# Kernel optimization log

Hardware: AMD Instinct MI355X
Metric: run time of the kernel (lower is better)

The kernel has to match this reference:

```python
import jax, jax.numpy as jnp
import numpy as np

D = 1024
D_H = 64

def setup_inputs() -> dict:
    key = jax.random.key(0)
    kx, kq, kk, kv = jax.random.split(key, 4)
    B, T = 4, 4096
    x = jax.random.normal(kx, (B, T, D), dtype=jnp.float32)
    # nn.Linear(d, d_H, bias=False) weights, stored as [d, d_H] (already transposed)
    s = 1.0 / np.sqrt(D)
    Wq = jax.random.uniform(kq, (D, D_H), dtype=jnp.float32, minval=-s, maxval=s)
    Wk = jax.random.uniform(kk, (D, D_H), dtype=jnp.float32, minval=-s, maxval=s)
    Wv = jax.random.uniform(kv, (D, D_H), dtype=jnp.float32, minval=-s, maxval=s)
    return {"x": x, "Wq": Wq, "Wk": Wk, "Wv": Wv}

def reference(x, Wq, Wk, Wv):
    B, T, d = x.shape
    Q = jnp.einsum('btd,dh->bth', x, Wq)
    K = jnp.einsum('btd,dh->bth', x, Wk)
    V = jnp.einsum('btd,dh->bth', x, Wv)
    # NOTE: original scales by self.d ** -0.5 (model dim), not d_H
    scores = jnp.einsum('bqh,bkh->bqk', Q, K) * (d ** -0.5)
    causal = jnp.tril(jnp.ones((T, T), dtype=bool))  # [T, T]
    scores = jnp.where(causal, scores, -jnp.inf)
    attn = jax.nn.softmax(scores, axis=-1)
    return jnp.einsum('bqk,bkh->bqh', attn, V)
```

## Files before the change

kernel.cpp:

```cpp
#include <hip/hip_runtime.h>
#include <hip/hip_bf16.h>

#define D_MODEL 1024
#define D_HEAD  64
#define T_SEQ   4096
#define NB      4
#define NROWS   (NB * T_SEQ)
#define SPLIT   8

typedef float f32x4 __attribute__((ext_vector_type(4)));
typedef __bf16 bf16x8 __attribute__((ext_vector_type(8)));
typedef unsigned short u16;

__device__ inline unsigned pk_bf16(float a, float b) {
    unsigned ua = __builtin_bit_cast(unsigned, a);
    unsigned ub = __builtin_bit_cast(unsigned, b);
    ua = (ua + 0x7FFFu + ((ua >> 16) & 1u)) >> 16;
    ub = (ub + 0x7FFFu + ((ub >> 16) & 1u)) >> 16;
    return ua | (ub << 16);
}
__device__ inline u16 bf16r(float a) {
    unsigned ua = __builtin_bit_cast(unsigned, a);
    return (u16)((ua + 0x7FFFu + ((ua >> 16) & 1u)) >> 16);
}

__global__ __launch_bounds__(256) void packw_kernel(
    const float* __restrict__ Wq, const float* __restrict__ Wk,
    const float* __restrict__ Wv, unsigned* __restrict__ Wpk)
{
    const int id = blockIdx.x * 256 + threadIdx.x;
    const int kb = id / 192;
    const int n  = id - kb * 192;
    const int sel = n >> 6, col = n & 63;
    const float* W = sel == 0 ? Wq : (sel == 1 ? Wk : Wv);
    float f[8];
#pragma unroll
    for (int j = 0; j < 8; ++j) f[j] = W[(kb * 8 + j) * 64 + col];
    uint4 o;
    o.x = pk_bf16(f[0], f[1]); o.y = pk_bf16(f[2], f[3]);
    o.z = pk_bf16(f[4], f[5]); o.w = pk_bf16(f[6], f[7]);
    *(uint4*)(Wpk + (size_t)id * 4) = o;
}

__global__ __launch_bounds__(256) void qkv_kernel(
    const float* __restrict__ x, const unsigned* __restrict__ Wpk,
    u16* __restrict__ Qbf, u16* __restrict__ Kbf, u16* __restrict__ Vt)
{
    __shared__ __align__(16) unsigned Xs[2][32 * 68];
    __shared__ __align__(16) u16 Vbuf[64 * 32];

    const int tid  = threadIdx.x;
    const int w    = tid >> 6;
    const int lane = tid & 63;
    const int nl   = lane & 15;
    const int quad = lane >> 4;
    const long row0 = (long)blockIdx.x * 32;

    const int srow = tid >> 5;
    const int scol = (tid & 31) * 4;

    f32x4 acc[2][3] = {};

    float4 nx[4];
#pragma unroll
    for (int p = 0; p < 4; ++p)
        nx[p] = *(const float4*)(x + (row0 + p * 8 + srow) * D_MODEL + scol);

    for (int ch = 0; ch < 8; ++ch) {
        const int buf = ch & 1;
#pragma unroll
        for (int p = 0; p < 4; ++p) {
            uint2 pk2;
            pk2.x = pk_bf16(nx[p].x, nx[p].y);
            pk2.y = pk_bf16(nx[p].z, nx[p].w);
            *(uint2*)&Xs[buf][(p * 8 + srow) * 68 + (scol >> 1)] = pk2;
        }
        __syncthreads();
        if (ch < 7) {
#pragma unroll
            for (int p = 0; p < 4; ++p)
                nx[p] = *(const float4*)(x + (row0 + p * 8 + srow) * D_MODEL
                                           + (ch + 1) * 128 + scol);
        }
#pragma unroll
        for (int kk = 0; kk < 4; ++kk) {
            const bf16x8 a0 = __builtin_bit_cast(bf16x8,
                *(const uint4*)&Xs[buf][nl * 68 + kk * 16 + quad * 4]);
            const bf16x8 a1 = __builtin_bit_cast(bf16x8,
                *(const uint4*)&Xs[buf][(16 + nl) * 68 + kk * 16 + quad * 4]);
            const unsigned* wb = Wpk + (size_t)(ch * 16 + kk * 4 + quad) * 768
                                     + (w * 48 + nl) * 4;
#pragma unroll
            for (int t = 0; t < 3; ++t) {
                const bf16x8 b = __builtin_bit_cast(bf16x8, *(const uint4*)(wb + t * 64));
                acc[0][t] = __builtin_amdgcn_mfma_f32_16x16x32_bf16(a0, b, acc[0][t], 0, 0, 0);
                acc[1][t] = __builtin_amdgcn_mfma_f32_16x16x32_bf16(a1, b, acc[1][t], 0, 0, 0);
            }
        }
        __syncthreads();
    }

    const float QSCALE = 0.04508422f;
#pragma unroll
    for (int t = 0; t < 3; ++t) {
        const int n0c = w * 48 + t * 16;
        const int sel = n0c >> 6;
        const int col = (n0c & 63) + nl;
#pragma unroll
        for (int m = 0; m < 2; ++m) {
            if (sel == 0) {
#pragma unroll
                for (int reg = 0; reg < 4; ++reg)
                    Qbf[(row0 + m * 16 + quad * 4 + reg) * D_HEAD + col] =
                        bf16r(acc[m][t][reg] * QSCALE);
            } else if (sel == 1) {
#pragma unroll
                for (int reg = 0; reg < 4; ++reg)
                    Kbf[(row0 + m * 16 + quad * 4 + reg) * D_HEAD + col] =
                        bf16r(acc[m][t][reg]);
            } else {
                uint2 p2;
                p2.x = pk_bf16(acc[m][t][0], acc[m][t][1]);
                p2.y = pk_bf16(acc[m][t][2], acc[m][t][3]);
                *(uint2*)&Vbuf[col * 32 + m * 16 + quad * 4] = p2;
            }
        }
    }
    __syncthreads();
    {
        const int dim  = tid >> 2;
        const int tseg = (tid & 3) * 8;
        const long bb   = row0 >> 12;
        const int tpos0 = (int)(row0 & 4095);
        const uint4 v = *(const uint4*)&Vbuf[dim * 32 + tseg];
        *(uint4*)&Vt[((bb * 64 + dim) << 12) + tpos0 + tseg] = v;
    }
}

__global__ __launch_bounds__(256, 3) void attn_kernel(
    const u16* __restrict__ Qbf, const u16* __restrict__ Kbf,
    const u16* __restrict__ Vt, u16* __restrict__ Po16, float* __restrict__ Pl)
{
    __shared__ __align__(16) u16 Pbuf[4][2][16 * 64];

    const int tid   = threadIdx.x;
    const int w     = tid >> 6;
    const int lane  = tid & 63;
    const int nl    = lane & 15;
    const int quad  = lane >> 4;
    const int gid   = blockIdx.x;
    const int b     = gid & 3;
    const int idx   = gid >> 2;
    const int half  = idx & 1;
    const int pair  = idx >> 1;
    const int sp    = half * 4 + w;

    const u16* Kb = Kbf + (size_t)b * T_SEQ * D_HEAD;
    const u16* Vb = Vt  + (size_t)b * D_HEAD * T_SEQ;

    const int tileA = 127 - pair;
    const int tileB = pair;
    const int nA = (tileA * 32 + 95) >> 6;
    const int nB = (tileB * 32 + 95) >> 6;
    const int cntA = (nA - sp + 7) >> 3;
    const int ktB0 = sp + 8 * cntA - nA;
    const int cntB = (ktB0 < nB) ? ((nB - ktB0 + 7) >> 3) : 0;

#define COMPUTEKV(kt_) do {                                                          \
    const int _k0 = (kt_) << 6;                                                      \
    uint4 buf[4][2];                                                                 \
    _Pragma("unroll") for (int t = 0; t < 4; ++t) {                                  \
        const u16* kp = Kb + (size_t)(_k0 + t * 16 + nl) * D_HEAD + quad * 8;        \
        buf[t][0] = *(const uint4*)kp;                                               \
        buf[t][1] = *(const uint4*)(kp + 32);                                        \
    }                                                                                \
    f32x4 S[2][4];                                                                   \
    _Pragma("unroll") for (int m = 0; m < 2; ++m)                                    \
    _Pragma("unroll") for (int t = 0; t < 4; ++t) {                                  \
        f32x4 z = {};                                                                \
        z = __builtin_amdgcn_mfma_f32_16x16x32_bf16(qf[m][0],                        \
                __builtin_bit_cast(bf16x8, buf[t][0]), z, 0, 0, 0);                  \
        S[m][t] = __builtin_amdgcn_mfma_f32_16x16x32_bf16(qf[m][1],                  \
                __builtin_bit_cast(bf16x8, buf[t][1]), z, 0, 0, 0);                  \
    }                                                                                \
    uint4 vbuf[4][2];               \
    _Pragma("unroll") for (int t = 0; t < 4; ++t) {                                  \
        const u16* vp = Vb + (size_t)(t * 16 + nl) * T_SEQ + _k0 + quad * 8;         \
        vbuf[t][0] = *(const uint4*)vp;                                              \
        vbuf[t][1] = *(const uint4*)(vp + 32);                                       \
    }                                                                                \
    _Pragma("unroll") for (int m = 0; m < 2; ++m) {                                  \
        const int _qb = wq0 + m * 16;                                                \
        if (_k0 + 63 > _qb) {                                                        \
            _Pragma("unroll") for (int t = 0; t < 4; ++t)                            \
            _Pragma("unroll") for (int reg = 0; reg < 4; ++reg)                      \
                if (_k0 + t * 16 + nl > _qb + quad * 4 + reg)                        \
                    S[m][t][reg] = -INFINITY;                                        \
        }                                                                            \
        _Pragma("unroll") for (int t = 0; t < 4; ++t)                                \
        _Pragma("unroll") for (int reg = 0; reg < 4; ++reg)                          \
            S[m][t][reg] = exp2f(S[m][t][reg]);                                      \
        _Pragma("unroll") for (int reg = 0; reg < 4; ++reg)                          \
            l[m][reg] += (S[m][0][reg] + S[m][1][reg])                               \
                       + (S[m][2][reg] + S[m][3][reg]);                              \
        u16* pb = Pbuf[w][m];                                                        \
        _Pragma("unroll") for (int t = 0; t < 4; ++t) {                              \
            const int g = 2 * t + (nl >> 3);                                         \
            _Pragma("unroll") for (int reg = 0; reg < 4; ++reg) {                    \
                const int q = quad * 4 + reg;                                        \
                pb[q * 64 + ((g ^ (q & 7)) * 8) + (nl & 7)] = bf16r(S[m][t][reg]);   \
            }                                                                        \
        }                                                                            \
    }                                                                                \
    _Pragma("unroll") for (int m = 0; m < 2; ++m) {                                  \
        const u16* pb = Pbuf[w][m];                                                  \
        const bf16x8 pf0 = __builtin_bit_cast(bf16x8,                                \
            *(const uint4*)&pb[nl * 64 + ((quad ^ (nl & 7)) * 8)]);                  \
        const bf16x8 pf1 = __builtin_bit_cast(bf16x8,                                \
            *(const uint4*)&pb[nl * 64 + (((4 + quad) ^ (nl & 7)) * 8)]);            \
        _Pragma("unroll") for (int t = 0; t < 4; ++t) {                              \
            Ot[m][t] = __builtin_amdgcn_mfma_f32_16x16x32_bf16(pf0,                  \
                        __builtin_bit_cast(bf16x8, vbuf[t][0]), Ot[m][t], 0, 0, 0);  \
            Ot[m][t] = __builtin_amdgcn_mfma_f32_16x16x32_bf16(pf1,                  \
                        __builtin_bit_cast(bf16x8, vbuf[t][1]), Ot[m][t], 0, 0, 0);  \
        }                                                                            \
    }                                                                                \
} while (0)

    auto runTile = [&](const int tile, const int kt0, const int cnt) {
        const int wq0 = tile * 32;

        bf16x8 qf[2][2];
#pragma unroll
        for (int m = 0; m < 2; ++m) {
            const u16* qp = Qbf + ((size_t)b * T_SEQ + wq0 + m * 16 + nl) * D_HEAD + quad * 8;
            qf[m][0] = __builtin_bit_cast(bf16x8, *(const uint4*)qp);
            qf[m][1] = __builtin_bit_cast(bf16x8, *(const uint4*)(qp + 32));
        }

        f32x4 Ot[2][4] = {};
        float l[2][4] = {{0.f,0.f,0.f,0.f},{0.f,0.f,0.f,0.f}};

        int kt = kt0;
        for (int i = 0; i < cnt; ++i, kt += 8)
            COMPUTEKV(kt);

#pragma unroll
        for (int m = 0; m < 2; ++m) {
#pragma unroll
            for (int reg = 0; reg < 4; ++reg) {
                float s = l[m][reg];
                s += __shfl_xor(s, 1);
                s += __shfl_xor(s, 2);
                s += __shfl_xor(s, 4);
                s += __shfl_xor(s, 8);
                l[m][reg] = s;
            }
            const int strip = tile * 2 + m;
            const int bs = b * 256 + strip;
            u16* po = Po16 + ((size_t)sp * 1024 + bs) * 1024;
#pragma unroll
            for (int t = 0; t < 4; ++t) {
                uint2 p2;
                p2.x = pk_bf16(Ot[m][t][0], Ot[m][t][1]);
                p2.y = pk_bf16(Ot[m][t][2], Ot[m][t][3]);
                *(uint2*)&po[(t * 16 + nl) * 16 + quad * 4] = p2;
            }
            if (nl == 0) {
                const size_t gr = (size_t)b * T_SEQ + wq0 + m * 16;
#pragma unroll
                for (int reg = 0; reg < 4; ++reg)
                    Pl[(size_t)sp * NROWS + gr + quad * 4 + reg] = l[m][reg];
            }
        }
    };

    runTile(tileA, sp,   cntA);
    runTile(tileB, ktB0, cntB);

#undef COMPUTEKV
}

__global__ __launch_bounds__(64) void reduce_kernel(
    const u16* __restrict__ Po16, const float* __restrict__ Pl,
    float* __restrict__ O)
{
    __shared__ float linv[16];
    const int bs    = blockIdx.x;
    const int b     = bs >> 8, strip = bs & 255;
    const size_t gr = (size_t)b * T_SEQ + strip * 16;
    const int c     = threadIdx.x;

    if (c < 16) {
        float s = 0.f;
#pragma unroll
        for (int sp = 0; sp < SPLIT; ++sp) s += Pl[(size_t)sp * NROWS + gr + c];
        linv[c] = 1.0f / s;
    }
    __syncthreads();

    float v[16] = {};
#pragma unroll
    for (int sp = 0; sp < SPLIT; ++sp) {
        const u16* p = Po16 + ((size_t)sp * 1024 + bs) * 1024 + c * 16;
        const uint4 x0 = *(const uint4*)p;
        const uint4 x1 = *(const uint4*)(p + 8);
        const unsigned uu[8] = {x0.x, x0.y, x0.z, x0.w, x1.x, x1.y, x1.z, x1.w};
#pragma unroll
        for (int i = 0; i < 8; ++i) {
            v[2*i]   += __builtin_bit_cast(float, uu[i] << 16);
            v[2*i+1] += __builtin_bit_cast(float, uu[i] & 0xFFFF0000u);
        }
    }
#pragma unroll
    for (int r = 0; r < 16; ++r)
        O[(gr + r) * D_HEAD + c] = v[r] * linv[r];
}

extern "C" void kernel_launch(void* const* d_in, const int* in_sizes, int n_in,
                              void* d_out, int out_size, void* d_ws, size_t ws_size,
                              hipStream_t stream) {
    const float* x  = (const float*)d_in[0];
    const float* Wq = (const float*)d_in[1];
    const float* Wk = (const float*)d_in[2];
    const float* Wv = (const float*)d_in[3];
    float* out = (float*)d_out;

    const size_t rows = NROWS;
    u16* Qbf = (u16*)d_ws;
    u16* Kbf = Qbf + rows * D_HEAD;
    u16* Vt  = Kbf + rows * D_HEAD;
    unsigned* Wpk = (unsigned*)(Vt + rows * D_HEAD);
    u16* Po16 = (u16*)(Wpk + 128 * 192 * 4);
    float* Pl = (float*)(Po16 + (size_t)SPLIT * rows * D_HEAD);

    hipLaunchKernelGGL(packw_kernel, dim3(96), dim3(256), 0, stream,
                       Wq, Wk, Wv, Wpk);
    hipLaunchKernelGGL(qkv_kernel, dim3(rows / 32), dim3(256), 0, stream,
                       x, Wpk, Qbf, Kbf, Vt);
    hipLaunchKernelGGL(attn_kernel, dim3(512), dim3(256), 0, stream,
                       Qbf, Kbf, Vt, Po16, Pl);
    hipLaunchKernelGGL(reduce_kernel, dim3(NB * 256), dim3(64), 0, stream,
                       Po16, Pl, out);
}
```

Measured before the change: 155.5 us.

## Prefetch next K tile in attention loop and parallelize split reduction

The attention inner loop is split into separate K-load, QK, softmax and PV stages. The next K tile is now prefetched while the current tile's second softmax and PV run, and a sched_barrier fixes the issue order. The projection kernel drops one of its two per-chunk barriers, which the double buffer allows. Input and partial-output traffic switches to nontemporal loads and stores. The reduce kernel now uses four waves that each sum two splits and combine through shared memory, trading more shared-memory use and register pressure for more memory-level parallelism.

```diff
diff --git a/kernel.cpp b/kernel.cpp
--- a/kernel.cpp
+++ b/kernel.cpp
@@ -11,6 +11,8 @@
 typedef float f32x4 __attribute__((ext_vector_type(4)));
 typedef __bf16 bf16x8 __attribute__((ext_vector_type(8)));
 typedef unsigned short u16;
+typedef unsigned u32x2 __attribute__((ext_vector_type(2)));
+typedef unsigned u32x4 __attribute__((ext_vector_type(4)));
 
 __device__ inline unsigned pk_bf16(float a, float b) {
     unsigned ua = __builtin_bit_cast(unsigned, a);
@@ -61,26 +63,28 @@
 
     f32x4 acc[2][3] = {};
 
-    float4 nx[4];
+    f32x4 nx[4];
 #pragma unroll
     for (int p = 0; p < 4; ++p)
-        nx[p] = *(const float4*)(x + (row0 + p * 8 + srow) * D_MODEL + scol);
+        nx[p] = __builtin_nontemporal_load(
+            (const f32x4*)(x + (row0 + p * 8 + srow) * D_MODEL + scol));
 
     for (int ch = 0; ch < 8; ++ch) {
         const int buf = ch & 1;
 #pragma unroll
         for (int p = 0; p < 4; ++p) {
             uint2 pk2;
-            pk2.x = pk_bf16(nx[p].x, nx[p].y);
-            pk2.y = pk_bf16(nx[p].z, nx[p].w);
+            pk2.x = pk_bf16(nx[p][0], nx[p][1]);
+            pk2.y = pk_bf16(nx[p][2], nx[p][3]);
             *(uint2*)&Xs[buf][(p * 8 + srow) * 68 + (scol >> 1)] = pk2;
         }
         __syncthreads();
         if (ch < 7) {
 #pragma unroll
             for (int p = 0; p < 4; ++p)
-                nx[p] = *(const float4*)(x + (row0 + p * 8 + srow) * D_MODEL
-                                           + (ch + 1) * 128 + scol);
+                nx[p] = __builtin_nontemporal_load(
+                    (const f32x4*)(x + (row0 + p * 8 + srow) * D_MODEL
+                                     + (ch + 1) * 128 + scol));
         }
 #pragma unroll
         for (int kk = 0; kk < 4; ++kk) {
@@ -97,8 +101,8 @@
                 acc[1][t] = __builtin_amdgcn_mfma_f32_16x16x32_bf16(a1, b, acc[1][t], 0, 0, 0);
             }
         }
-        __syncthreads();
-    }
+    }
+    __syncthreads();
 
     const float QSCALE = 0.04508422f;
 #pragma unroll
@@ -163,67 +167,71 @@
     const int nA = (tileA * 32 + 95) >> 6;
     const int nB = (tileB * 32 + 95) >> 6;
     const int cntA = (nA - sp + 7) >> 3;
-    const int ktB0 = sp + 8 * cntA - nA;
+    const int ktB0 = sp + SPLIT * cntA - nA;
     const int cntB = (ktB0 < nB) ? ((nB - ktB0 + 7) >> 3) : 0;
 
-#define COMPUTEKV(kt_) do {                                                          \
-    const int _k0 = (kt_) << 6;                                                      \
-    uint4 buf[4][2];                                                                 \
-    _Pragma("unroll") for (int t = 0; t < 4; ++t) {                                  \
-        const u16* kp = Kb + (size_t)(_k0 + t * 16 + nl) * D_HEAD + quad * 8;        \
-        buf[t][0] = *(const uint4*)kp;                                               \
-        buf[t][1] = *(const uint4*)(kp + 32);                                        \
-    }                                                                                \
-    f32x4 S[2][4];                                                                   \
-    _Pragma("unroll") for (int m = 0; m < 2; ++m)                                    \
-    _Pragma("unroll") for (int t = 0; t < 4; ++t) {                                  \
-        f32x4 z = {};                                                                \
-        z = __builtin_amdgcn_mfma_f32_16x16x32_bf16(qf[m][0],                        \
-                __builtin_bit_cast(bf16x8, buf[t][0]), z, 0, 0, 0);                  \
-        S[m][t] = __builtin_amdgcn_mfma_f32_16x16x32_bf16(qf[m][1],                  \
-                __builtin_bit_cast(bf16x8, buf[t][1]), z, 0, 0, 0);                  \
-    }                                                                                \
-    uint4 vbuf[4][2];               \
-    _Pragma("unroll") for (int t = 0; t < 4; ++t) {                                  \
-        const u16* vp = Vb + (size_t)(t * 16 + nl) * T_SEQ + _k0 + quad * 8;         \
+#define LOADK(kt_) do {                                                              \
+    const int _kk0 = (kt_) << 6;                                                     \
+    _Pragma("unroll") for (int t = 0; t < 4; ++t) {                                  \
+        const u16* kp = Kb + (size_t)(_kk0 + t * 16 + nl) * D_HEAD + quad * 8;       \
+        kbuf[t][0] = *(const uint4*)kp;                                              \
+        kbuf[t][1] = *(const uint4*)(kp + 32);                                       \
+    }                                                                                \
+} while (0)
+
+#define LOADV(kt_) do {                                                              \
+    const int _kv0 = (kt_) << 6;                                                     \
+    _Pragma("unroll") for (int t = 0; t < 4; ++t) {                                  \
+        const u16* vp = Vb + (size_t)(t * 16 + nl) * T_SEQ + _kv0 + quad * 8;        \
         vbuf[t][0] = *(const uint4*)vp;                                              \
         vbuf[t][1] = *(const uint4*)(vp + 32);                                       \
     }                                                                                \
-    _Pragma("unroll") for (int m = 0; m < 2; ++m) {                                  \
-        const int _qb = wq0 + m * 16;                                                \
-        if (_k0 + 63 > _qb) {                                                        \
-            _Pragma("unroll") for (int t = 0; t < 4; ++t)                            \
-            _Pragma("unroll") for (int reg = 0; reg < 4; ++reg)                      \
-                if (_k0 + t * 16 + nl > _qb + quad * 4 + reg)                        \
-                    S[m][t][reg] = -INFINITY;                                        \
-        }                                                                            \
+} while (0)
+
+#define QK_M(m_, Sd_) do {                                                           \
+    _Pragma("unroll") for (int t = 0; t < 4; ++t) {                                  \
+        f32x4 z = {};                                                                \
+        z = __builtin_amdgcn_mfma_f32_16x16x32_bf16(qf[m_][0],                       \
+                __builtin_bit_cast(bf16x8, kbuf[t][0]), z, 0, 0, 0);                 \
+        Sd_[t] = __builtin_amdgcn_mfma_f32_16x16x32_bf16(qf[m_][1],                  \
+                __builtin_bit_cast(bf16x8, kbuf[t][1]), z, 0, 0, 0);                 \
+    }                                                                                \
+} while (0)
+
+#define SMAX_M(m_, Sd_) do {                                                         \
+    const int _qb = wq0 + (m_) * 16;                                                 \
+    if (k0c + 63 > _qb) {                                                            \
         _Pragma("unroll") for (int t = 0; t < 4; ++t)                                \
         _Pragma("unroll") for (int reg = 0; reg < 4; ++reg)                          \
-            S[m][t][reg] = exp2f(S[m][t][reg]);                                      \
-        _Pragma("unroll") for (int reg = 0; reg < 4; ++reg)                          \
-            l[m][reg] += (S[m][0][reg] + S[m][1][reg])                               \
-                       + (S[m][2][reg] + S[m][3][reg]);                              \
-        u16* pb = Pbuf[w][m];                                                        \
-        _Pragma("unroll") for (int t = 0; t < 4; ++t) {                              \
-            const int g = 2 * t + (nl >> 3);                                         \
-            _Pragma("unroll") for (int reg = 0; reg < 4; ++reg) {                    \
-                const int q = quad * 4 + reg;                                        \
-                pb[q * 64 + ((g ^ (q & 7)) * 8) + (nl & 7)] = bf16r(S[m][t][reg]);   \
-            }                                                                        \
+            if (k0c + t * 16 + nl > _qb + quad * 4 + reg)                            \
+                Sd_[t][reg] = -INFINITY;                                             \
+    }                                                                                \
+    _Pragma("unroll") for (int t = 0; t < 4; ++t)                                    \
+    _Pragma("unroll") for (int reg = 0; reg < 4; ++reg)                              \
+        Sd_[t][reg] = exp2f(Sd_[t][reg]);                                            \
+    _Pragma("unroll") for (int reg = 0; reg < 4; ++reg)                              \
+        l[m_][reg] += (Sd_[0][reg] + Sd_[1][reg]) + (Sd_[2][reg] + Sd_[3][reg]);     \
+    u16* pb = Pbuf[w][m_];                                                           \
+    _Pragma("unroll") for (int t = 0; t < 4; ++t) {                                  \
+        const int g = 2 * t + (nl >> 3);                                             \
+        _Pragma("unroll") for (int reg = 0; reg < 4; ++reg) {                        \
+            const int q = quad * 4 + reg;                                            \
+            pb[q * 64 + ((g ^ (q & 7)) * 8) + (nl & 7)] = bf16r(Sd_[t][reg]);        \
         }                                                                            \
     }                                                                                \
-    _Pragma("unroll") for (int m = 0; m < 2; ++m) {                                  \
-        const u16* pb = Pbuf[w][m];                                                  \
-        const bf16x8 pf0 = __builtin_bit_cast(bf16x8,                                \
-            *(const uint4*)&pb[nl * 64 + ((quad ^ (nl & 7)) * 8)]);                  \
-        const bf16x8 pf1 = __builtin_bit_cast(bf16x8,                                \
-            *(const uint4*)&pb[nl * 64 + (((4 + quad) ^ (nl & 7)) * 8)]);            \
-        _Pragma("unroll") for (int t = 0; t < 4; ++t) {                              \
-            Ot[m][t] = __builtin_amdgcn_mfma_f32_16x16x32_bf16(pf0,                  \
-                        __builtin_bit_cast(bf16x8, vbuf[t][0]), Ot[m][t], 0, 0, 0);  \
-            Ot[m][t] = __builtin_amdgcn_mfma_f32_16x16x32_bf16(pf1,                  \
-                        __builtin_bit_cast(bf16x8, vbuf[t][1]), Ot[m][t], 0, 0, 0);  \
-        }                                                                            \
+} while (0)
+
+#define PV_M(m_) do {                                                                \
+    const u16* pb = Pbuf[w][m_];                                                     \
+    const bf16x8 pf0 = __builtin_bit_cast(bf16x8,                                    \
+        *(const uint4*)&pb[nl * 64 + ((quad ^ (nl & 7)) * 8)]);                      \
+    const bf16x8 pf1 = __builtin_bit_cast(bf16x8,                                    \
+        *(const uint4*)&pb[nl * 64 + (((4 + quad) ^ (nl & 7)) * 8)]);                \
+    _Pragma("unroll") for (int t = 0; t < 4; ++t) {                                  \
+        Ot[m_][t] = __builtin_amdgcn_mfma_f32_16x16x32_bf16(pf0,                     \
+                    __builtin_bit_cast(bf16x8, vbuf[t][0]), Ot[m_][t], 0, 0, 0);     \
+        Ot[m_][t] = __builtin_amdgcn_mfma_f32_16x16x32_bf16(pf1,                     \
+                    __builtin_bit_cast(bf16x8, vbuf[t][1]), Ot[m_][t], 0, 0, 0);     \
     }                                                                                \
 } while (0)
 
@@ -241,9 +249,22 @@
         f32x4 Ot[2][4] = {};
         float l[2][4] = {{0.f,0.f,0.f,0.f},{0.f,0.f,0.f,0.f}};
 
+        uint4 kbuf[4][2], vbuf[4][2];
+        if (cnt > 0) LOADK(kt0);
         int kt = kt0;
-        for (int i = 0; i < cnt; ++i, kt += 8)
-            COMPUTEKV(kt);
+        for (int i = 0; i < cnt; ++i, kt += SPLIT) {
+            const int k0c = kt << 6;
+            f32x4 S0[4], S1[4];
+            QK_M(0, S0);
+            SMAX_M(0, S0);
+            QK_M(1, S1);
+            LOADV(kt);
+            __builtin_amdgcn_sched_barrier(0);
+            if (i + 1 < cnt) LOADK(kt + SPLIT);
+            SMAX_M(1, S1);
+            PV_M(0);
+            PV_M(1);
+        }
 
 #pragma unroll
         for (int m = 0; m < 2; ++m) {
@@ -261,16 +282,17 @@
             u16* po = Po16 + ((size_t)sp * 1024 + bs) * 1024;
 #pragma unroll
             for (int t = 0; t < 4; ++t) {
-                uint2 p2;
-                p2.x = pk_bf16(Ot[m][t][0], Ot[m][t][1]);
-                p2.y = pk_bf16(Ot[m][t][2], Ot[m][t][3]);
-                *(uint2*)&po[(t * 16 + nl) * 16 + quad * 4] = p2;
+                u32x2 p2;
+                p2[0] = pk_bf16(Ot[m][t][0], Ot[m][t][1]);
+                p2[1] = pk_bf16(Ot[m][t][2], Ot[m][t][3]);
+                __builtin_nontemporal_store(p2, (u32x2*)&po[(t * 16 + nl) * 16 + quad * 4]);
             }
             if (nl == 0) {
                 const size_t gr = (size_t)b * T_SEQ + wq0 + m * 16;
 #pragma unroll
                 for (int reg = 0; reg < 4; ++reg)
-                    Pl[(size_t)sp * NROWS + gr + quad * 4 + reg] = l[m][reg];
+                    __builtin_nontemporal_store(l[m][reg],
+                        &Pl[(size_t)sp * NROWS + gr + quad * 4 + reg]);
             }
         }
     };
@@ -278,43 +300,56 @@
     runTile(tileA, sp,   cntA);
     runTile(tileB, ktB0, cntB);
 
-#undef COMPUTEKV
-}
-
-__global__ __launch_bounds__(64) void reduce_kernel(
+#undef LOADK
+#undef LOADV
+#undef QK_M
+#undef SMAX_M
+#undef PV_M
+}
+
+__global__ __launch_bounds__(256) void reduce_kernel(
     const u16* __restrict__ Po16, const float* __restrict__ Pl,
     float* __restrict__ O)
 {
+    __shared__ float part[4][16][64];
+    __shared__ float lsum[4][16];
     __shared__ float linv[16];
-    const int bs    = blockIdx.x;
-    const int b     = bs >> 8, strip = bs & 255;
+    const int tid = threadIdx.x;
+    const int w   = tid >> 6;
+    const int c   = tid & 63;
+    const int bs  = blockIdx.x;
+    const int b   = bs >> 8, strip = bs & 255;
     const size_t gr = (size_t)b * T_SEQ + strip * 16;
-    const int c     = threadIdx.x;
-
-    if (c < 16) {
-        float s = 0.f;
-#pragma unroll
-        for (int sp = 0; sp < SPLIT; ++sp) s += Pl[(size_t)sp * NROWS + gr + c];
-        linv[c] = 1.0f / s;
-    }
+
+    float v[16] = {};
+    float ls = 0.f;
+#pragma unroll
+    for (int i = 0; i < 2; ++i) {
+        const int sp = w + i * 4;
+        const u16* p = Po16 + ((size_t)sp * 1024 + bs) * 1024 + c * 16;
+        const u32x4 x0 = __builtin_nontemporal_load((const u32x4*)p);
+        const u32x4 x1 = __builtin_nontemporal_load((const u32x4*)p + 1);
+        const unsigned uu[8] = {x0[0], x0[1], x0[2], x0[3], x1[0], x1[1], x1[2], x1[3]};
+#pragma unroll
+        for (int j = 0; j < 8; ++j) {
+            v[2*j]   += __builtin_bit_cast(float, uu[j] << 16);
+            v[2*j+1] += __builtin_bit_cast(float, uu[j] & 0xFFFF0000u);
+        }
+        if (c < 16) ls += Pl[(size_t)sp * NROWS + gr + c];
+    }
+#pragma unroll
+    for (int r = 0; r < 16; ++r) part[w][r][c] = v[r];
+    if (c < 16) lsum[w][c] = ls;
     __syncthreads();
-
-    float v[16] = {};
-#pragma unroll
-    for (int sp = 0; sp < SPLIT; ++sp) {
-        const u16* p = Po16 + ((size_t)sp * 1024 + bs) * 1024 + c * 16;
-        const uint4 x0 = *(const uint4*)p;
-        const uint4 x1 = *(const uint4*)(p + 8);
-        const unsigned uu[8] = {x0.x, x0.y, x0.z, x0.w, x1.x, x1.y, x1.z, x1.w};
-#pragma unroll
-        for (int i = 0; i < 8; ++i) {
-            v[2*i]   += __builtin_bit_cast(float, uu[i] << 16);
-            v[2*i+1] += __builtin_bit_cast(float, uu[i] & 0xFFFF0000u);
-        }
-    }
-#pragma unroll
-    for (int r = 0; r < 16; ++r)
-        O[(gr + r) * D_HEAD + c] = v[r] * linv[r];
+    if (tid < 16)
+        linv[tid] = 1.0f / (lsum[0][tid] + lsum[1][tid] + lsum[2][tid] + lsum[3][tid]);
+    __syncthreads();
+#pragma unroll
+    for (int j = 0; j < 4; ++j) {
+        const int r = w + j * 4;
+        const float s = (part[0][r][c] + part[1][r][c]) + (part[2][r][c] + part[3][r][c]);
+        O[(gr + r) * D_HEAD + c] = s * linv[r];
+    }
 }
 
 extern "C" void kernel_launch(void* const* d_in, const int* in_sizes, int n_in,
@@ -340,6 +375,6 @@
                        x, Wpk, Qbf, Kbf, Vt);
     hipLaunchKernelGGL(attn_kernel, dim3(512), dim3(256), 0, stream,
                        Qbf, Kbf, Vt, Po16, Pl);
-    hipLaunchKernelGGL(reduce_kernel, dim3(NB * 256), dim3(64), 0, stream,
+    hipLaunchKernelGGL(reduce_kernel, dim3(NB * 256), dim3(64 * 4), 0, stream,
                        Po16, Pl, out);
 }
```

Measured after the change: 200.5 us. 1.29x slower.

## Halve QKV row tile, drop loop barrier, parallelize split reduction across waves

Applied to the files above, without the earlier changes.

The QKV projection kernel now handles 16 rows per block instead of 32, which doubles the grid. It also drops the trailing barrier inside the K loop, relying on the double-buffered shared tile for safety. The reduce kernel now uses four waves per strip: each wave sums two splits, and the partials are combined through shared memory. Attention partial outputs and row sums are written, and read back in the reduce kernel, with nontemporal hints. The intent is more parallelism and fewer syncs in the smaller kernels. The cost is that each QKV block reuses its weights across fewer rows, so it does more weight loads per row.

```diff
diff --git a/kernel.cpp b/kernel.cpp
--- a/kernel.cpp
+++ b/kernel.cpp
@@ -11,6 +11,8 @@
 typedef float f32x4 __attribute__((ext_vector_type(4)));
 typedef __bf16 bf16x8 __attribute__((ext_vector_type(8)));
 typedef unsigned short u16;
+typedef unsigned u32x2 __attribute__((ext_vector_type(2)));
+typedef unsigned u32x4 __attribute__((ext_vector_type(4)));
 
 __device__ inline unsigned pk_bf16(float a, float b) {
     unsigned ua = __builtin_bit_cast(unsigned, a);
@@ -46,59 +48,56 @@
     const float* __restrict__ x, const unsigned* __restrict__ Wpk,
     u16* __restrict__ Qbf, u16* __restrict__ Kbf, u16* __restrict__ Vt)
 {
-    __shared__ __align__(16) unsigned Xs[2][32 * 68];
-    __shared__ __align__(16) u16 Vbuf[64 * 32];
+    __shared__ __align__(16) unsigned Xs[2][16 * 68];
+    __shared__ __align__(16) u16 Vbuf[64 * 16];
 
     const int tid  = threadIdx.x;
     const int w    = tid >> 6;
     const int lane = tid & 63;
     const int nl   = lane & 15;
     const int quad = lane >> 4;
-    const long row0 = (long)blockIdx.x * 32;
+    const long row0 = (long)blockIdx.x * 16;
 
     const int srow = tid >> 5;
     const int scol = (tid & 31) * 4;
 
-    f32x4 acc[2][3] = {};
-
-    float4 nx[4];
-#pragma unroll
-    for (int p = 0; p < 4; ++p)
-        nx[p] = *(const float4*)(x + (row0 + p * 8 + srow) * D_MODEL + scol);
+    f32x4 acc[3] = {};
+
+    f32x4 nx[2];
+#pragma unroll
+    for (int p = 0; p < 2; ++p)
+        nx[p] = *(const f32x4*)(x + (row0 + p * 8 + srow) * D_MODEL + scol);
 
     for (int ch = 0; ch < 8; ++ch) {
         const int buf = ch & 1;
 #pragma unroll
-        for (int p = 0; p < 4; ++p) {
+        for (int p = 0; p < 2; ++p) {
             uint2 pk2;
-            pk2.x = pk_bf16(nx[p].x, nx[p].y);
-            pk2.y = pk_bf16(nx[p].z, nx[p].w);
+            pk2.x = pk_bf16(nx[p][0], nx[p][1]);
+            pk2.y = pk_bf16(nx[p][2], nx[p][3]);
             *(uint2*)&Xs[buf][(p * 8 + srow) * 68 + (scol >> 1)] = pk2;
         }
         __syncthreads();
         if (ch < 7) {
 #pragma unroll
-            for (int p = 0; p < 4; ++p)
-                nx[p] = *(const float4*)(x + (row0 + p * 8 + srow) * D_MODEL
-                                           + (ch + 1) * 128 + scol);
+            for (int p = 0; p < 2; ++p)
+                nx[p] = *(const f32x4*)(x + (row0 + p * 8 + srow) * D_MODEL
+                                          + (ch + 1) * 128 + scol);
         }
 #pragma unroll
         for (int kk = 0; kk < 4; ++kk) {
             const bf16x8 a0 = __builtin_bit_cast(bf16x8,
                 *(const uint4*)&Xs[buf][nl * 68 + kk * 16 + quad * 4]);
-            const bf16x8 a1 = __builtin_bit_cast(bf16x8,
-                *(const uint4*)&Xs[buf][(16 + nl) * 68 + kk * 16 + quad * 4]);
             const unsigned* wb = Wpk + (size_t)(ch * 16 + kk * 4 + quad) * 768
                                      + (w * 48 + nl) * 4;
 #pragma unroll
             for (int t = 0; t < 3; ++t) {
                 const bf16x8 b = __builtin_bit_cast(bf16x8, *(const uint4*)(wb + t * 64));
-                acc[0][t] = __builtin_amdgcn_mfma_f32_16x16x32_bf16(a0, b, acc[0][t], 0, 0, 0);
-                acc[1][t] = __builtin_amdgcn_mfma_f32_16x16x32_bf16(a1, b, acc[1][t], 0, 0, 0);
+                acc[t] = __builtin_amdgcn_mfma_f32_16x16x32_bf16(a0, b, acc[t], 0, 0, 0);
             }
         }
-        __syncthreads();
-    }
+    }
+    __syncthreads();
 
     const float QSCALE = 0.04508422f;
 #pragma unroll
@@ -106,34 +105,31 @@
         const int n0c = w * 48 + t * 16;
         const int sel = n0c >> 6;
         const int col = (n0c & 63) + nl;
-#pragma unroll
-        for (int m = 0; m < 2; ++m) {
-            if (sel == 0) {
-#pragma unroll
-                for (int reg = 0; reg < 4; ++reg)
-                    Qbf[(row0 + m * 16 + quad * 4 + reg) * D_HEAD + col] =
-                        bf16r(acc[m][t][reg] * QSCALE);
-            } else if (sel == 1) {
-#pragma unroll
-                for (int reg = 0; reg < 4; ++reg)
-                    Kbf[(row0 + m * 16 + quad * 4 + reg) * D_HEAD + col] =
-                        bf16r(acc[m][t][reg]);
-            } else {
-                uint2 p2;
-                p2.x = pk_bf16(acc[m][t][0], acc[m][t][1]);
-                p2.y = pk_bf16(acc[m][t][2], acc[m][t][3]);
-                *(uint2*)&Vbuf[col * 32 + m * 16 + quad * 4] = p2;
-            }
+        if (sel == 0) {
+#pragma unroll
+            for (int reg = 0; reg < 4; ++reg)
+                Qbf[(row0 + quad * 4 + reg) * D_HEAD + col] =
+                    bf16r(acc[t][reg] * QSCALE);
+        } else if (sel == 1) {
+#pragma unroll
+            for (int reg = 0; reg < 4; ++reg)
+                Kbf[(row0 + quad * 4 + reg) * D_HEAD + col] =
+                    bf16r(acc[t][reg]);
+        } else {
+            uint2 p2;
+            p2.x = pk_bf16(acc[t][0], acc[t][1]);
+            p2.y = pk_bf16(acc[t][2], acc[t][3]);
+            *(uint2*)&Vbuf[col * 16 + quad * 4] = p2;
         }
     }
     __syncthreads();
     {
         const int dim  = tid >> 2;
-        const int tseg = (tid & 3) * 8;
+        const int tseg = (tid & 3) * 4;
         const long bb   = row0 >> 12;
         const int tpos0 = (int)(row0 & 4095);
-        const uint4 v = *(const uint4*)&Vbuf[dim * 32 + tseg];
-        *(uint4*)&Vt[((bb * 64 + dim) << 12) + tpos0 + tseg] = v;
+        const uint2 v = *(const uint2*)&Vbuf[dim * 16 + tseg];
+        *(uint2*)&Vt[((bb * 64 + dim) << 12) + tpos0 + tseg] = v;
     }
 }
 
@@ -163,7 +159,7 @@
     const int nA = (tileA * 32 + 95) >> 6;
     const int nB = (tileB * 32 + 95) >> 6;
     const int cntA = (nA - sp + 7) >> 3;
-    const int ktB0 = sp + 8 * cntA - nA;
+    const int ktB0 = sp + SPLIT * cntA - nA;
     const int cntB = (ktB0 < nB) ? ((nB - ktB0 + 7) >> 3) : 0;
 
 #define COMPUTEKV(kt_) do {                                                          \
@@ -242,7 +238,7 @@
         float l[2][4] = {{0.f,0.f,0.f,0.f},{0.f,0.f,0.f,0.f}};
 
         int kt = kt0;
-        for (int i = 0; i < cnt; ++i, kt += 8)
+        for (int i = 0; i < cnt; ++i, kt += SPLIT)
             COMPUTEKV(kt);
 
 #pragma unroll
@@ -261,16 +257,17 @@
             u16* po = Po16 + ((size_t)sp * 1024 + bs) * 1024;
 #pragma unroll
             for (int t = 0; t < 4; ++t) {
-                uint2 p2;
-                p2.x = pk_bf16(Ot[m][t][0], Ot[m][t][1]);
-                p2.y = pk_bf16(Ot[m][t][2], Ot[m][t][3]);
-                *(uint2*)&po[(t * 16 + nl) * 16 + quad * 4] = p2;
+                u32x2 p2;
+                p2[0] = pk_bf16(Ot[m][t][0], Ot[m][t][1]);
+                p2[1] = pk_bf16(Ot[m][t][2], Ot[m][t][3]);
+                __builtin_nontemporal_store(p2, (u32x2*)&po[(t * 16 + nl) * 16 + quad * 4]);
             }
             if (nl == 0) {
                 const size_t gr = (size_t)b * T_SEQ + wq0 + m * 16;
 #pragma unroll
                 for (int reg = 0; reg < 4; ++reg)
-                    Pl[(size_t)sp * NROWS + gr + quad * 4 + reg] = l[m][reg];
+                    __builtin_nontemporal_store(l[m][reg],
+                        &Pl[(size_t)sp * NROWS + gr + quad * 4 + reg]);
             }
         }
     };
@@ -281,40 +278,49 @@
 #undef COMPUTEKV
 }
 
-__global__ __launch_bounds__(64) void reduce_kernel(
+__global__ __launch_bounds__(256) void reduce_kernel(
     const u16* __restrict__ Po16, const float* __restrict__ Pl,
     float* __restrict__ O)
 {
+    __shared__ float part[4][16][64];
+    __shared__ float lsum[4][16];
     __shared__ float linv[16];
-    const int bs    = blockIdx.x;
-    const int b     = bs >> 8, strip = bs & 255;
+    const int tid = threadIdx.x;
+    const int w   = tid >> 6;
+    const int c   = tid & 63;
+    const int bs  = blockIdx.x;
+    const int b   = bs >> 8, strip = bs & 255;
     const size_t gr = (size_t)b * T_SEQ + strip * 16;
-    const int c     = threadIdx.x;
-
-    if (c < 16) {
-        float s = 0.f;
-#pragma unroll
-        for (int sp = 0; sp < SPLIT; ++sp) s += Pl[(size_t)sp * NROWS + gr + c];
-        linv[c] = 1.0f / s;
-    }
+
+    float v[16] = {};
+    float ls = 0.f;
+#pragma unroll
+    for (int i = 0; i < 2; ++i) {
+        const int sp = w + i * 4;
+        const u16* p = Po16 + ((size_t)sp * 1024 + bs) * 1024 + c * 16;
+        const u32x4 x0 = __builtin_nontemporal_load((const u32x4*)p);
+        const u32x4 x1 = __builtin_nontemporal_load((const u32x4*)p + 1);
+        const unsigned uu[8] = {x0[0], x0[1], x0[2], x0[3], x1[0], x1[1], x1[2], x1[3]};
+#pragma unroll
+        for (int j = 0; j < 8; ++j) {
+            v[2*j]   += __builtin_bit_cast(float, uu[j] << 16);
+            v[2*j+1] += __builtin_bit_cast(float, uu[j] & 0xFFFF0000u);
+        }
+        if (c < 16) ls += Pl[(size_t)sp * NROWS + gr + c];
+    }
+#pragma unroll
+    for (int r = 0; r < 16; ++r) part[w][r][c] = v[r];
+    if (c < 16) lsum[w][c] = ls;
     __syncthreads();
-
-    float v[16] = {};
-#pragma unroll
-    for (int sp = 0; sp < SPLIT; ++sp) {
-        const u16* p = Po16 + ((size_t)sp * 1024 + bs) * 1024 + c * 16;
-        const uint4 x0 = *(const uint4*)p;
-        const uint4 x1 = *(const uint4*)(p + 8);
-        const unsigned uu[8] = {x0.x, x0.y, x0.z, x0.w, x1.x, x1.y, x1.z, x1.w};
-#pragma unroll
-        for (int i = 0; i < 8; ++i) {
-            v[2*i]   += __builtin_bit_cast(float, uu[i] << 16);
-            v[2*i+1] += __builtin_bit_cast(float, uu[i] & 0xFFFF0000u);
-        }
-    }
-#pragma unroll
-    for (int r = 0; r < 16; ++r)
-        O[(gr + r) * D_HEAD + c] = v[r] * linv[r];
+    if (tid < 16)
+        linv[tid] = 1.0f / (lsum[0][tid] + lsum[1][tid] + lsum[2][tid] + lsum[3][tid]);
+    __syncthreads();
+#pragma unroll
+    for (int j = 0; j < 4; ++j) {
+        const int r = w + j * 4;
+        const float s = (part[0][r][c] + part[1][r][c]) + (part[2][r][c] + part[3][r][c]);
+        O[(gr + r) * D_HEAD + c] = s * linv[r];
+    }
 }
 
 extern "C" void kernel_launch(void* const* d_in, const int* in_sizes, int n_in,
@@ -336,10 +342,10 @@
 
     hipLaunchKernelGGL(packw_kernel, dim3(96), dim3(256), 0, stream,
                        Wq, Wk, Wv, Wpk);
-    hipLaunchKernelGGL(qkv_kernel, dim3(rows / 32), dim3(256), 0, stream,
+    hipLaunchKernelGGL(qkv_kernel, dim3(rows / 16), dim3(256), 0, stream,
                        x, Wpk, Qbf, Kbf, Vt);
     hipLaunchKernelGGL(attn_kernel, dim3(512), dim3(256), 0, stream,
                        Qbf, Kbf, Vt, Po16, Pl);
-    hipLaunchKernelGGL(reduce_kernel, dim3(NB * 256), dim3(64), 0, stream,
+    hipLaunchKernelGGL(reduce_kernel, dim3(NB * 256), dim3(64 * 4), 0, stream,
                        Po16, Pl, out);
 }
```

Result: slower. 159.7 us (+2.7%).
